# Performance work log

Hardware: AMD Instinct MI355X
Metric: run time of the kernel (lower is better)

The kernel has to match this reference:

```python
import jax, jax.numpy as jnp
import numpy as np

B, G, GI = 128, 360, 174          # batch, n_groups, voxels per group
EF, ET, U = 512, 512, 512         # feat embed, text embed, LSTM units
AU, VOC, T = 32, 5000, 20         # attention units, vocab, max_len


def _leaky(x):
    return jnp.where(x >= 0, x, 0.2 * x)


def _ln(x, g, b, eps=1e-5):
    m = x.mean(-1, keepdims=True)
    v = ((x - m) ** 2).mean(-1, keepdims=True)
    return (x - m) / jnp.sqrt(v + eps) * g + b


def setup_inputs() -> dict:
    key = jax.random.key(0)
    ks = jax.random.split(key, 24)
    def n(k, shape, s=0.02):
        return jax.random.normal(k, shape, jnp.float32) * s
    return {
        "features": jax.random.normal(ks[0], (B, G * GI), jnp.float32),
        "text": jax.random.randint(ks[1], (B, T), 0, VOC),
        "a0": jnp.zeros((B, U), jnp.float32),
        "c0": jnp.zeros((B, U), jnp.float32),
        "enc_W": n(ks[2], (G, GI, EF)), "enc_b": n(ks[3], (G, EF)),
        "enc_ln_g": jnp.ones((EF,), jnp.float32), "enc_ln_b": jnp.zeros((EF,), jnp.float32),
        "attn_W1": n(ks[4], (EF, AU)), "attn_b1": n(ks[5], (AU,)),
        "attn_W2": n(ks[6], (U, AU)), "attn_b2": n(ks[7], (AU,)),
        "attn_V": n(ks[8], (AU, 1)), "attn_bV": n(ks[9], (1,)),
        "emb": n(ks[10], (VOC, ET)),
        "W_ih": n(ks[11], (4 * U, EF + ET)), "W_hh": n(ks[12], (4 * U, U)),
        "b_ih": n(ks[13], (4 * U,)), "b_hh": n(ks[14], (4 * U,)),
        "ln_g": jnp.ones((U,), jnp.float32), "ln_b": jnp.zeros((U,), jnp.float32),
        "dec_W1": n(ks[15], (U, 256)), "dec_b1": n(ks[16], (256,)),
        "dec_W2": n(ks[17], (256, VOC)), "dec_b2": n(ks[18], (VOC,)),
        "subject": 0,
    }


def reference(features, text, a0, c0, enc_W, enc_b, enc_ln_g, enc_ln_b,
              attn_W1, attn_b1, attn_W2, attn_b2, attn_V, attn_bV, emb,
              W_ih, W_hh, b_ih, b_hh, ln_g, ln_b,
              dec_W1, dec_b1, dec_W2, dec_b2, subject):
    # LocallyConnected encoder (weights for the selected subject): groups are
    # 360 contiguous equal splits of the voxel axis -> gather == reshape.
    x = features.reshape(B, G, GI)
    feat = _ln(_leaky(jnp.einsum('bgi,gio->bgo', x, enc_W) + enc_b),
               enc_ln_g, enc_ln_b)                       # [B, G, EF]
    # hidden-independent half of attention, hoisted out of the recurrence
    f1 = jax.nn.relu(jnp.einsum('bge,eu->bgu', feat, attn_W1) + attn_b1)  # [B,G,AU]
    txt = emb[text]                                      # [B, T, ET]

    def step(carry, x_t):
        a, c = carry                                     # [B,U], [B,U]
        h2 = jax.nn.relu(a @ attn_W2 + attn_b2)          # [B, AU]
        score = jnp.tanh(f1 + h2[:, None, :]) @ attn_V + attn_bV  # [B,G,1]
        w = jax.nn.softmax(score, axis=1)
        ctx = jnp.sum(w * feat, axis=1)                  # [B, EF]
        xin = jnp.concatenate([ctx, x_t], axis=1)        # [B, EF+ET]
        gates = xin @ W_ih.T + a @ W_hh.T + b_ih + b_hh  # [B, 4U]
        i, f, g, o = jnp.split(gates, 4, axis=1)         # torch gate order i,f,g,o
        c = jax.nn.sigmoid(f) * c + jax.nn.sigmoid(i) * jnp.tanh(g)
        h = jax.nn.sigmoid(o) * jnp.tanh(c)
        a = _ln(_leaky(h), ln_g, ln_b)                   # fed back as LSTM hidden
        out = jax.nn.softmax(_leaky(a @ dec_W1 + dec_b1) @ dec_W2 + dec_b2, axis=-1)
        return (a, c), (out, w)

    _, (outs, ws) = jax.lax.scan(step, (a0, c0), jnp.swapaxes(txt, 0, 1))
    output = jnp.swapaxes(outs, 0, 1)                    # [B, T, VOC]
    attention_scores = jnp.swapaxes(ws, 0, 1)            # [B, T, G, 1]
    return output, attention_scores
```

## Files before the change

### kernel.cpp

```cpp
#include <hip/hip_runtime.h>
#include <stdint.h>

#define B_  128
#define G_  360
#define GI_ 174
#define EF_ 512
#define U_  512
#define AU_ 32
#define VOC_ 5000
#define T_  20

typedef short short8 __attribute__((ext_vector_type(8)));
typedef float floatx4 __attribute__((ext_vector_type(4)));

#define GLD16(gp, lp) __builtin_amdgcn_global_load_lds( \
    (const __attribute__((address_space(1))) void*)(gp), \
    (__attribute__((address_space(3))) void*)(lp), 16, 0, 0)

__device__ __forceinline__ unsigned short f2bf(float f){
  unsigned u = __float_as_uint(f);
  u += 0x7fffu + ((u>>16)&1u);
  return (unsigned short)(u>>16);
}
__device__ __forceinline__ float2 bfpair(unsigned u){
  float2 r; r.x = __uint_as_float(u<<16); r.y = __uint_as_float(u & 0xffff0000u); return r;
}
__device__ __forceinline__ unsigned packbf(float a, float b){
  return ((unsigned)f2bf(b)<<16) | (unsigned)f2bf(a);
}
__device__ __forceinline__ float sigmf(float x){ return 1.0f/(1.0f + __expf(-x)); }
__device__ __forceinline__ float tanhf_(float x){ return 1.0f - 2.0f/(1.0f + __expf(2.0f*x)); }
__device__ __forceinline__ float leaky_(float x){ return x >= 0.f ? x : 0.2f*x; }

__device__ __forceinline__ int swzcol(int cc, int e){
  return (cc & ~63) | ((((cc>>3)&7) ^ e)<<3) | (cc&7);
}

__global__ __launch_bounds__(256) void k_cvt(
    const int* __restrict__ text, const float* __restrict__ emb,
    const float* __restrict__ Wih, const float* __restrict__ Whh,
    const float* __restrict__ bih, const float* __restrict__ bhh,
    const float* __restrict__ W1, const float* __restrict__ b1,
    const float* __restrict__ encg, const float* __restrict__ encb,
    const float* __restrict__ dW1, const float* __restrict__ dW2,
    float* __restrict__ stats, unsigned short* __restrict__ Wstep,
    float* __restrict__ bias_sum, unsigned short* __restrict__ ASbuf,
    unsigned short* __restrict__ W1g, float* __restrict__ f1c,
    unsigned short* __restrict__ dW1t, unsigned short* __restrict__ dW2t)
{
  __shared__ float tile[64][65];
  const int blk = blockIdx.x, tid = threadIdx.x;
  if (blk < 90){
    int i = blk*1024 + tid*4;
    *(float4*)&stats[i] = make_float4(0.f,0.f,0.f,0.f);
  } else if (blk < 346){
    int j = (blk - 90)*8 + (tid >> 5);
    int e = j & 7;
    #pragma unroll
    for (int z=0; z<6; ++z){
      int c0 = ((tid & 31) + 32*z)*8;
      float4 v0, v1;
      if (c0 < 512){
        v0 = *(const float4*)&Wih[(size_t)j*1024 + 512 + c0];
        v1 = *(const float4*)&Wih[(size_t)j*1024 + 512 + c0 + 4];
      } else if (c0 < 1024){
        v0 = *(const float4*)&Wih[(size_t)j*1024 + (c0 - 512)];
        v1 = *(const float4*)&Wih[(size_t)j*1024 + (c0 - 512) + 4];
      } else {
        v0 = *(const float4*)&Whh[(size_t)j*512 + (c0 - 1024)];
        v1 = *(const float4*)&Whh[(size_t)j*512 + (c0 - 1024) + 4];
      }
      uint4 pk;
      pk.x = packbf(v0.x, v0.y); pk.y = packbf(v0.z, v0.w);
      pk.z = packbf(v1.x, v1.y); pk.w = packbf(v1.z, v1.w);
      int cd0;
      if (c0 < 512) cd0 = c0;
      else {
        int cc = c0 - 512;
        cd0 = 512 + ((cc & ~63) | ((((cc>>3)&7) ^ e)<<3));
      }
      *(uint4*)&Wstep[(size_t)j*1536 + cd0] = pk;
    }
  } else if (blk < 354){
    int i = (blk-346)*256 + tid;
    bias_sum[i] = bih[i] + bhh[i];
  } else if (blk < 2914){
    int r = blk - 354; int t = r >> 7, b = r & 127;
    int idx = text[b*T_ + t];
    float2 v = *(const float2*)&emb[(size_t)idx*512 + 2*tid];
    ((unsigned*)ASbuf)[(((size_t)r*1536)>>1) + tid] = packbf(v.x, v.y);
  } else if (blk == 2914){
    if (tid < 32){
      float gw = 0.f, bw = 0.f;
      for (int k=0;k<512;++k){
        float wv = W1[(size_t)k*32 + tid];
        float gk = encg[k], bk = encb[k];
        W1g[(size_t)tid*512 + k] = f2bf(gk*wv);
        gw += gk*wv; bw += bk*wv;
      }
      f1c[tid] = gw; f1c[32+tid] = bw + b1[tid];
    }
  } else if (blk < 2947){
    int q = blk - 2915; int kt = q >> 2, nt = q & 3;
    int k0 = kt*64, n0 = nt*64;
    #pragma unroll
    for (int it=0; it<16; ++it){
      int idx = it*256 + tid; int kk = idx>>6, nn = idx&63;
      tile[kk][nn] = dW1[(size_t)(k0+kk)*256 + n0+nn];
    }
    __syncthreads();
    #pragma unroll
    for (int it=0; it<16; ++it){
      int idx = it*256 + tid; int nn = idx>>6, kk = idx&63;
      dW1t[(size_t)(n0+nn)*512 + k0+kk] = f2bf(tile[kk][nn]);
    }
  } else {
    int q = blk - 2947; int kt = q/80, nt = q - kt*80;
    int k0 = kt*64, n0 = nt*64;
    #pragma unroll
    for (int it=0; it<16; ++it){
      int idx = it*256 + tid; int kk = idx>>6, nn = idx&63;
      tile[kk][nn] = (n0+nn < VOC_) ? dW2[(size_t)(k0+kk)*VOC_ + n0+nn] : 0.f;
    }
    __syncthreads();
    #pragma unroll
    for (int it=0; it<16; ++it){
      int idx = it*256 + tid; int nn = idx>>6, kk = idx&63;
      dW2t[(size_t)(n0+nn)*256 + k0+kk] = f2bf(tile[kk][nn]);
    }
  }
}

__device__ __forceinline__ int swz64(int row, int k){
  return row*64 + ((((k>>3) ^ (row&7)))<<3) + (k&7);
}
__global__ __launch_bounds__(256) void k_enc(
    const float* __restrict__ features, const float* __restrict__ encW,
    const float* __restrict__ encB,
    unsigned short* __restrict__ ybuf, float* __restrict__ stats)
{
  __shared__ __align__(16) unsigned short As[64*64];
  __shared__ __align__(16) unsigned short Bs[64*64];
  const int g = blockIdx.y;
  const int m0 = (blockIdx.x >> 3)*64, n0 = (blockIdx.x & 7)*64;
  const int tid = threadIdx.x, w = tid>>6, l = tid&63;
  const int quad = l>>4, col16 = l&15;
  const int m0w = (w>>1)*32, n0w = (w&1)*32;

  floatx4 acc[2][2];
  #pragma unroll
  for (int mi=0;mi<2;++mi)
    #pragma unroll
    for (int ni=0;ni<2;++ni)
      acc[mi][ni] = (floatx4){0.f,0.f,0.f,0.f};

  for (int c=0; c<3; ++c){
    if (c > 0) __syncthreads();
    #pragma unroll
    for (int q=0; q<4; ++q){
      int idx = q*256 + tid;
      int row = idx >> 4;
      int kl  = (idx & 15)*4;
      int kgl = c*64 + kl;
      const float* fp = features + (size_t)(m0+row)*(G_*GI_) + (size_t)g*GI_ + kgl;
      float4 v;
      if (kgl + 3 < GI_){
        v = *(const float4*)fp;
      } else {
        v.x = (kgl+0 < GI_) ? fp[0] : 0.f;
        v.y = (kgl+1 < GI_) ? fp[1] : 0.f;
        v.z = (kgl+2 < GI_) ? fp[2] : 0.f;
        v.w = (kgl+3 < GI_) ? fp[3] : 0.f;
      }
      int e = row*64 + (((kl>>3) ^ (row&7))<<3) + (kl&7);
      uint2 pk; pk.x = packbf(v.x, v.y); pk.y = packbf(v.z, v.w);
      *(uint2*)&As[e] = pk;
    }
    #pragma unroll
    for (int z=0; z<8; ++z){
      int kk = (tid>>5) + 8*z;
      int k  = c*64 + kk;
      int nn = (tid&31)*2;
      if (k < GI_){
        const float* wp = encW + ((size_t)g*GI_ + k)*512 + n0 + nn;
        float2 v = *(const float2*)wp;
        Bs[swz64(nn,   kk)] = f2bf(v.x);
        Bs[swz64(nn+1, kk)] = f2bf(v.y);
      } else {
        Bs[swz64(nn,   kk)] = 0;
        Bs[swz64(nn+1, kk)] = 0;
      }
    }
    __syncthreads();
    #pragma unroll
    for (int it=0; it<2; ++it){
      int kk = it*32 + quad*8;
      short8 af[2], bfr[2];
      #pragma unroll
      for (int mi=0;mi<2;++mi){
        int row = m0w + mi*16 + col16;
        af[mi] = *(const short8*)&As[row*64 + (((kk>>3) ^ (row&7))<<3)];
      }
      #pragma unroll
      for (int ni=0;ni<2;++ni){
        int rowb = n0w + ni*16 + col16;
        bfr[ni] = *(const short8*)&Bs[rowb*64 + (((kk>>3) ^ (rowb&7))<<3)];
      }
      #pragma unroll
      for (int mi=0;mi<2;++mi)
        #pragma unroll
        for (int ni=0;ni<2;++ni)
          acc[mi][ni] = __builtin_amdgcn_mfma_f32_16x16x32_bf16(af[mi], bfr[ni], acc[mi][ni], 0,0,0);
    }
  }

  #pragma unroll
  for (int mi=0;mi<2;++mi){
    float sy[4] = {0.f,0.f,0.f,0.f};
    float sq[4] = {0.f,0.f,0.f,0.f};
    #pragma unroll
    for (int ni=0;ni<2;++ni){
      int nG = n0 + n0w + ni*16 + col16;
      float bv = encB[(size_t)g*512 + nG];
      #pragma unroll
      for (int reg=0;reg<4;++reg){
        int row = m0 + m0w + mi*16 + quad*4 + reg;
        float y = leaky_(acc[mi][ni][reg] + bv);
        unsigned short yh = f2bf(y);
        ybuf[((size_t)row*G_ + g)*512 + nG] = yh;
        float yr = __uint_as_float(((unsigned)yh)<<16);
        sy[reg] += yr; sq[reg] += yr*yr;
      }
    }
    #pragma unroll
    for (int reg=0; reg<4; ++reg){
      float a = sy[reg], bq = sq[reg];
      #pragma unroll
      for (int mk=1; mk<16; mk<<=1){ a += __shfl_xor(a, mk, 64); bq += __shfl_xor(bq, mk, 64); }
      if (col16 == 0){
        int row = m0 + m0w + mi*16 + quad*4 + reg;
        atomicAdd(&stats[((size_t)row*G_ + g)*2],     a);
        atomicAdd(&stats[((size_t)row*G_ + g)*2 + 1], bq);
      }
    }
  }
}

template<int TN, int NBK, int MODE, int KSPLIT=1>
__global__ __launch_bounds__(256) void k_gemm(
    const unsigned short* __restrict__ A, int lda,
    const unsigned short* __restrict__ Bt, int ldb,
    const float* __restrict__ bias,
    float* __restrict__ outf, unsigned short* __restrict__ outh,
    const float* __restrict__ stats, float* __restrict__ stats2,
    const float* __restrict__ f1c)
{
  constexpr int NI = TN/32;
  __shared__ __align__(16) unsigned short As[128*64];
  __shared__ __align__(16) unsigned short Bs[TN*64];
  const int tid = threadIdx.x;
  const int w = tid >> 6, l = tid & 63;
  const int n0 = blockIdx.x * TN;
  const int ks = (KSPLIT > 1) ? blockIdx.y : 0;
  const int r0 = (KSPLIT > 1) ? 0 : blockIdx.y * 128;
  const int quad = l>>4, col16 = l&15;
  const int m0w = (w>>1)*64, n0w = (w&1)*(TN/2);
  const int arow = w*32, brow = w*(TN/4);

  const unsigned short* Ag = A + (size_t)(r0 + arow + (l>>3))*lda + (l&7)*8;
  const unsigned short* Bg = Bt + (size_t)(n0 + brow + (l>>3))*ldb + (l&7)*8;

  floatx4 acc[4][NI];
  #pragma unroll
  for (int mi=0;mi<4;++mi)
    #pragma unroll
    for (int ni=0;ni<NI;++ni)
      acc[mi][ni] = (floatx4){0.f,0.f,0.f,0.f};

  for (int it=0; it<NBK; ++it){
    int k0 = (ks*NBK + it)*64;
    #pragma unroll
    for (int q=0;q<4;++q)
      GLD16(Ag + (size_t)q*8*lda + k0, As + (arow + q*8)*64);
    #pragma unroll
    for (int q=0;q<TN/32;++q)
      GLD16(Bg + (size_t)q*8*ldb + k0, Bs + (brow + q*8)*64);
    __syncthreads();
    #pragma unroll
    for (int kc=0;kc<2;++kc){
      int koff = kc*32 + quad*8;
      short8 af[4], bfr[NI];
      #pragma unroll
      for (int mi=0;mi<4;++mi)
        af[mi] = *(const short8*)&As[(m0w + mi*16 + col16)*64 + koff];
      #pragma unroll
      for (int ni=0;ni<NI;++ni)
        bfr[ni] = *(const short8*)&Bs[(n0w + ni*16 + col16)*64 + koff];
      #pragma unroll
      for (int mi=0;mi<4;++mi)
        #pragma unroll
        for (int ni=0;ni<NI;++ni)
          acc[mi][ni] = __builtin_amdgcn_mfma_f32_16x16x32_bf16(af[mi], bfr[ni], acc[mi][ni], 0,0,0);
    }
    __syncthreads();
  }

  if constexpr (MODE == 0){
    float* op = outf + (size_t)ks*(128*2048);
    #pragma unroll
    for (int ni=0; ni<NI; ++ni){
      int nG = n0 + n0w + ni*16 + col16;
      float bv = (KSPLIT == 1 || ks == 0) ? bias[nG] : 0.f;
      #pragma unroll
      for (int mi=0; mi<4; ++mi)
        #pragma unroll
        for (int reg=0; reg<4; ++reg){
          int r = r0 + m0w + mi*16 + quad*4 + reg;
          op[(size_t)r*2048 + nG] = acc[mi][ni][reg] + bv;
        }
    }
  } else if constexpr (MODE == 1){
    int nG = n0w + col16;
    float gw = f1c[nG], bwv = f1c[32+nG];
    #pragma unroll
    for (int mi=0; mi<4; ++mi)
      #pragma unroll
      for (int reg=0; reg<4; ++reg){
        int r = r0 + m0w + mi*16 + quad*4 + reg;
        float2 st = *(const float2*)&stats[(size_t)r*2];
        float m = st.x * (1.f/512.f);
        float var = st.y * (1.f/512.f) - m*m;
        float rs = rsqrtf(var + 1e-5f);
        float v = rs*(acc[mi][0][reg] - m*gw) + bwv;
        v = v > 0.f ? v : 0.f;
        outf[(size_t)r*32 + nG] = v;
        if (((w&1)==0) && col16==0){
          stats2[(size_t)r*2] = m; stats2[(size_t)r*2+1] = rs;
        }
      }
  } else if constexpr (MODE == 2){
    #pragma unroll
    for (int ni=0; ni<NI; ++ni){
      int nG = n0 + n0w + ni*16 + col16;
      float bv = bias[nG];
      #pragma unroll
      for (int mi=0; mi<4; ++mi)
        #pragma unroll
        for (int reg=0; reg<4; ++reg){
          int r = r0 + m0w + mi*16 + quad*4 + reg;
          outh[(size_t)r*256 + nG] = f2bf(leaky_(acc[mi][ni][reg] + bv));
        }
    }
  } else {
    #pragma unroll
    for (int ni=0; ni<NI; ++ni){
      int nG = n0 + n0w + ni*16 + col16;
      if (nG < VOC_){
        float bv = bias[nG];
        #pragma unroll
        for (int mi=0; mi<4; ++mi)
          #pragma unroll
          for (int reg=0; reg<4; ++reg){
            int r = r0 + m0w + mi*16 + quad*4 + reg;
            int bb = r & 127, tt = r >> 7;
            outf[((size_t)bb*T_ + tt)*VOC_ + nG] = acc[mi][ni][reg] + bv;
          }
      }
    }
  }
}

__global__ __launch_bounds__(256) void k_gates(
    const unsigned short* __restrict__ A,
    const unsigned short* __restrict__ Bt,
    float* __restrict__ outp)
{
  __shared__ __align__(16) unsigned short As[128*128];
  __shared__ __align__(16) unsigned short Bs[64*128];
  const int tid = threadIdx.x, w = tid>>6, l = tid&63;
  const int ks = blockIdx.y;
  const int n0 = blockIdx.x*64;
  const int quad = l>>4, col16 = l&15;
  const int m0w = (w>>1)*64, n0w = (w&1)*32;
  const int arow = w*32, brow = w*16;

  const unsigned short* Ag = A + (size_t)(arow + (l>>4))*1536 + ks*128 + (l&15)*8;
  const unsigned short* Bg = Bt + (size_t)(n0 + brow + (l>>4))*1536 + 512 + ks*128 + (l&15)*8;
  #pragma unroll
  for (int q=0;q<8;++q)
    GLD16(Ag + (size_t)q*4*1536, As + (arow + q*4)*128);
  #pragma unroll
  for (int q=0;q<4;++q)
    GLD16(Bg + (size_t)q*4*1536, Bs + (brow + q*4)*128);

  floatx4 acc[4][2];
  #pragma unroll
  for (int mi=0;mi<4;++mi)
    #pragma unroll
    for (int ni=0;ni<2;++ni)
      acc[mi][ni] = (floatx4){0.f,0.f,0.f,0.f};

  __syncthreads();
  #pragma unroll
  for (int kc=0;kc<4;++kc){
    int koff = kc*32 + quad*8;
    int kbase = koff & 64;
    int kx = (koff>>3)&7;
    short8 af[4], bfr[2];
    #pragma unroll
    for (int mi=0;mi<4;++mi){
      int row = m0w + mi*16 + col16;
      af[mi] = *(const short8*)&As[row*128 + kbase + ((kx ^ (row&7))<<3)];
    }
    #pragma unroll
    for (int ni=0;ni<2;++ni){
      int rowb = n0w + ni*16 + col16;
      bfr[ni] = *(const short8*)&Bs[rowb*128 + kbase + ((kx ^ (rowb&7))<<3)];
    }
    #pragma unroll
    for (int mi=0;mi<4;++mi)
      #pragma unroll
      for (int ni=0;ni<2;++ni)
        acc[mi][ni] = __builtin_amdgcn_mfma_f32_16x16x32_bf16(af[mi], bfr[ni], acc[mi][ni], 0,0,0);
  }

  float* op = outp + (size_t)ks*(128*2048);
  #pragma unroll
  for (int ni=0; ni<2; ++ni){
    int nG = n0 + n0w + ni*16 + col16;
    #pragma unroll
    for (int mi=0; mi<4; ++mi)
      #pragma unroll
      for (int reg=0; reg<4; ++reg){
        int r = m0w + mi*16 + quad*4 + reg;
        op[(size_t)r*2048 + nG] = acc[mi][ni][reg];
      }
  }
}

__global__ __launch_bounds__(256) void k_cellattn(
    const float* __restrict__ gall, const float* __restrict__ gtx,
    const float* __restrict__ c_in,
    float* __restrict__ c_out, const float* __restrict__ a0,
    const float* __restrict__ lng, const float* __restrict__ lnb,
    const float* __restrict__ W2, const float* __restrict__ b2,
    const float* __restrict__ Vv, const float* __restrict__ bV,
    const float* __restrict__ f1, const unsigned short* __restrict__ ybuf,
    const float* __restrict__ stats2,
    const float* __restrict__ encg, const float* __restrict__ encb,
    unsigned short* __restrict__ ASlot, unsigned short* __restrict__ a_bf,
    float* __restrict__ att_out, int t_att, int mode_cell, int do_attn)
{
  __shared__ float a_s[512];
  __shared__ float sc[G_];
  __shared__ float hred[8*32];
  __shared__ float h2s[32];
  __shared__ float red[16];
  __shared__ float mrs[2];
  __shared__ float2 cred[4][256];
  const int b = blockIdx.x, tid = threadIdx.x;
  const int wv = tid >> 6, ln = tid & 63;

  if (mode_cell){
    float hl2[2];
    #pragma unroll
    for (int q=0;q<2;++q){
      int u = tid + q*256;
      size_t base = (size_t)b*2048;
      float gi = gtx[base+u];
      float gf = gtx[base+512+u];
      float gc = gtx[base+1024+u];
      float go = gtx[base+1536+u];
      #pragma unroll
      for (int s=0;s<8;++s){
        const float* gp = gall + (size_t)s*(128*2048) + base;
        gi += gp[u]; gf += gp[512+u]; gc += gp[1024+u]; go += gp[1536+u];
      }
      float c = sigmf(gf)*c_in[(size_t)b*512+u] + sigmf(gi)*tanhf_(gc);
      c_out[(size_t)b*512+u] = c;
      hl2[q] = leaky_(sigmf(go)*tanhf_(c));
    }
    float s = hl2[0]+hl2[1], ss = hl2[0]*hl2[0]+hl2[1]*hl2[1];
    #pragma unroll
    for (int mk=1;mk<64;mk<<=1){ s += __shfl_xor(s,mk,64); ss += __shfl_xor(ss,mk,64); }
    if (ln==0){ red[wv]=s; red[8+wv]=ss; }
    __syncthreads();
    if (tid==0){
      float S  = red[0]+red[1]+red[2]+red[3];
      float SS = red[8]+red[9]+red[10]+red[11];
      float mean = S*(1.f/512.f);
      float var  = SS*(1.f/512.f) - mean*mean;
      mrs[0]=mean; mrs[1]=rsqrtf(var+1e-5f);
    }
    __syncthreads();
    float mean = mrs[0], rstd = mrs[1];
    #pragma unroll
    for (int q=0;q<2;++q){
      int u = tid + q*256;
      float av = (hl2[q]-mean)*rstd*lng[u] + lnb[u];
      a_s[u] = av;
      a_bf[(size_t)b*512 + u] = f2bf(av);
      if (do_attn){
        int pc = swzcol(512 + u, b&7);
        ASlot[(size_t)b*1536 + 512 + pc] = f2bf(av);
      }
    }
  } else {
    #pragma unroll
    for (int q=0;q<2;++q){
      int u = tid + q*256;
      float av = a0[(size_t)b*512 + u];
      a_s[u] = av;
      int pc = swzcol(512 + u, b&7);
      ASlot[(size_t)b*1536 + 512 + pc] = f2bf(av);
    }
  }
  __syncthreads();
  if (!do_attn) return;

  {
    int u = tid & 31, ch = tid >> 5;
    float p = 0.f;
    const float* w2p = W2 + (size_t)ch*64*32 + u;
    const float* ap = a_s + ch*64;
    #pragma unroll 8
    for (int e=0;e<64;++e) p += ap[e]*w2p[(size_t)e*32];
    hred[ch*32+u] = p;
  }
  __syncthreads();
  if (tid < 32){
    float p = hred[tid];
    #pragma unroll
    for (int ch=1; ch<8; ++ch) p += hred[ch*32+tid];
    p += b2[tid];
    h2s[tid] = p>0.f? p:0.f;
  }
  __syncthreads();
  float bVv = bV[0];
  for (int gg = tid; gg < G_; gg += 256){
    const float* fp = f1 + ((size_t)b*G_ + gg)*32;
    float s = bVv;
    #pragma unroll
    for (int u=0;u<32;++u) s += tanhf_(fp[u] + h2s[u]) * Vv[u];
    sc[gg] = s;
  }
  __syncthreads();
  float mx = -1e30f;
  for (int gg=tid; gg<G_; gg+=256) mx = fmaxf(mx, sc[gg]);
  #pragma unroll
  for (int mk=1;mk<64;mk<<=1) mx = fmaxf(mx, __shfl_xor(mx,mk,64));
  if (ln==0) red[wv]=mx;
  __syncthreads();
  if (tid==0) red[0] = fmaxf(fmaxf(red[0],red[1]),fmaxf(red[2],red[3]));
  __syncthreads();
  mx = red[0];
  float psum = 0.f;
  for (int gg=tid; gg<G_; gg+=256){
    float e = __expf(sc[gg]-mx);
    sc[gg] = e; psum += e;
  }
  #pragma unroll
  for (int mk=1;mk<64;mk<<=1) psum += __shfl_xor(psum,mk,64);
  if (ln==0) red[8+wv]=psum;
  __syncthreads();
  if (tid==0) red[8] = red[8]+red[9]+red[10]+red[11];
  __syncthreads();
  float inv = 1.f/red[8];
  float Mop = 0.f;
  float* wout = att_out + ((size_t)b*T_ + t_att)*G_;
  for (int gg=tid; gg<G_; gg+=256){
    float wg = sc[gg]*inv;
    wout[gg] = wg;
    float2 st = *(const float2*)&stats2[((size_t)b*G_+gg)*2];
    sc[gg] = wg*st.y;
    Mop += wg*st.x*st.y;
  }
  #pragma unroll
  for (int mk=1;mk<64;mk<<=1) Mop += __shfl_xor(Mop,mk,64);
  if (ln==0) red[4+wv] = Mop;
  __syncthreads();
  if (tid==0) mrs[0] = red[4]+red[5]+red[6]+red[7];
  __syncthreads();
  float Mo = mrs[0];
  {
    const unsigned* fp = (const unsigned*)ybuf + ((size_t)b*G_)*256;
    float2 cacc[4];
    #pragma unroll
    for (int k=0;k<4;++k) cacc[k] = make_float2(0.f,0.f);
    int g0 = wv*90;
    for (int gg=g0; gg<g0+90; ++gg){
      float wq = sc[gg];
      #pragma unroll
      for (int k=0;k<4;++k){
        float2 p = bfpair(fp[(size_t)gg*256 + ln + 64*k]);
        cacc[k].x += wq*p.x; cacc[k].y += wq*p.y;
      }
    }
    #pragma unroll
    for (int k=0;k<4;++k) cred[wv][ln + 64*k] = cacc[k];
  }
  __syncthreads();
  {
    float c0v = cred[0][tid].x + cred[1][tid].x + cred[2][tid].x + cred[3][tid].x;
    float c1v = cred[0][tid].y + cred[1][tid].y + cred[2][tid].y + cred[3][tid].y;
    int e0 = 2*tid;
    float ctx0 = encg[e0]  *(c0v - Mo) + encb[e0];
    float ctx1 = encg[e0+1]*(c1v - Mo) + encb[e0+1];
    int pc = swzcol(2*tid, b&7);
    ((unsigned*)ASlot)[((size_t)b*1536 + 512 + pc)>>1] = packbf(ctx0, ctx1);
  }
}

__global__ __launch_bounds__(256) void k_softmax(float* __restrict__ outp)
{
  __shared__ float red[8];
  const size_t row = (size_t)blockIdx.x * VOC_;
  const int tid = threadIdx.x;
  const int wv = tid >> 6, ln = tid & 63;
  float v[20];
  float mx = -1e30f;
  #pragma unroll
  for (int k=0;k<20;++k){
    int idx = tid + k*256;
    v[k] = (idx < VOC_) ? outp[row+idx] : -1e30f;
    mx = fmaxf(mx, v[k]);
  }
  #pragma unroll
  for (int mk=1;mk<64;mk<<=1) mx = fmaxf(mx,__shfl_xor(mx,mk,64));
  if (ln==0) red[wv] = mx;
  __syncthreads();
  if (tid==0) red[0]=fmaxf(fmaxf(red[0],red[1]),fmaxf(red[2],red[3]));
  __syncthreads();
  mx = red[0];
  float s=0.f;
  #pragma unroll
  for (int k=0;k<20;++k){ v[k] = __expf(v[k]-mx); s += v[k]; }
  #pragma unroll
  for (int mk=1;mk<64;mk<<=1) s += __shfl_xor(s,mk,64);
  if (ln==0) red[4+wv]=s;
  __syncthreads();
  if (tid==0) red[4]=red[4]+red[5]+red[6]+red[7];
  __syncthreads();
  float inv = 1.f/red[4];
  #pragma unroll
  for (int k=0;k<20;++k){
    int idx = tid + k*256;
    if (idx < VOC_) outp[row+idx] = v[k]*inv;
  }
}

extern "C" void kernel_launch(void* const* d_in, const int* in_sizes, int n_in,
                              void* d_out, int out_size, void* d_ws, size_t ws_size,
                              hipStream_t stream) {
  const float* features = (const float*)d_in[0];
  const int*   text     = (const int*)d_in[1];
  const float* a0    = (const float*)d_in[2];
  const float* c0    = (const float*)d_in[3];
  const float* encW  = (const float*)d_in[4];
  const float* encB  = (const float*)d_in[5];
  const float* encLNg= (const float*)d_in[6];
  const float* encLNb= (const float*)d_in[7];
  const float* attnW1= (const float*)d_in[8];
  const float* attnb1= (const float*)d_in[9];
  const float* attnW2= (const float*)d_in[10];
  const float* attnb2= (const float*)d_in[11];
  const float* attnV = (const float*)d_in[12];
  const float* attnbV= (const float*)d_in[13];
  const float* emb   = (const float*)d_in[14];
  const float* Wih   = (const float*)d_in[15];
  const float* Whh   = (const float*)d_in[16];
  const float* bih   = (const float*)d_in[17];
  const float* bhh   = (const float*)d_in[18];
  const float* lng   = (const float*)d_in[19];
  const float* lnb   = (const float*)d_in[20];
  const float* dW1   = (const float*)d_in[21];
  const float* db1   = (const float*)d_in[22];
  const float* dW2   = (const float*)d_in[23];
  const float* db2   = (const float*)d_in[24];

  uint8_t* w8 = (uint8_t*)d_ws;
  unsigned short* ybuf   = (unsigned short*)(w8);
  float*          stats  = (float*)(w8 + 47185920);
  float*          stats2 = (float*)(w8 + 47554560);
  float*          f1b    = (float*)(w8 + 47923200);
  unsigned short* ASbuf  = (unsigned short*)(w8 + 53821440);
  unsigned short* Wstep  = (unsigned short*)(w8 + 61685760);
  float*          bias_sum=(float*)(w8 + 67977216);
  unsigned short* W1g    = (unsigned short*)(w8 + 67985408);
  float*          f1c    = (float*)(w8 + 68018176);
  unsigned short* dW1t   = (unsigned short*)(w8 + 68018432);
  unsigned short* dW2t   = (unsigned short*)(w8 + 68280576);
  float*          cws    = (float*)(w8 + 71950592);
  unsigned short* a_bf   = (unsigned short*)(w8 + 72212736);
  unsigned short* d1bf   = (unsigned short*)(w8 + 74834176);

  float* outp = (float*)d_out;
  float* att  = outp + 12800000;
  float* gsplit = outp;
  float* gtxt   = outp + 8*128*2048;

  hipLaunchKernelGGL(k_cvt, dim3(3267), dim3(256), 0, stream,
                     text, emb, Wih, Whh, bih, bhh, attnW1, attnb1,
                     encLNg, encLNb, dW1, dW2,
                     stats, Wstep, bias_sum, ASbuf, W1g, f1c, dW1t, dW2t);
  hipLaunchKernelGGL(k_enc, dim3(16,360), dim3(256), 0, stream,
                     features, encW, encB, ybuf, stats);
  hipLaunchKernelGGL((k_gemm<64,8,0>), dim3(32,20), dim3(256), 0, stream,
                     ASbuf, 1536, Wstep, 1536, bias_sum,
                     gtxt, (unsigned short*)nullptr,
                     (const float*)nullptr, (float*)nullptr, (const float*)nullptr);
  hipLaunchKernelGGL((k_gemm<32,8,1>), dim3(1,360), dim3(256), 0, stream,
                     ybuf, 512, W1g, 512, (const float*)nullptr,
                     f1b, (unsigned short*)nullptr, stats, stats2, f1c);
  hipLaunchKernelGGL(k_cellattn, dim3(128), dim3(256), 0, stream,
                     gsplit, gtxt, c0, cws, a0, lng, lnb, attnW2, attnb2, attnV, attnbV,
                     f1b, ybuf, stats2, encLNg, encLNb,
                     ASbuf, a_bf, att, 0, 0, 1);
  for (int t=0; t<T_; ++t){
    hipLaunchKernelGGL(k_gates, dim3(32,8), dim3(256), 0, stream,
                       ASbuf + (size_t)t*128*1536 + 512, Wstep, gsplit);
    int da = (t < T_-1) ? 1 : 0;
    unsigned short* slot = ASbuf + (size_t)((t+1 < T_) ? (t+1) : 0)*128*1536;
    hipLaunchKernelGGL(k_cellattn, dim3(128), dim3(256), 0, stream,
                       gsplit, gtxt + (size_t)t*128*2048, (t==0)?c0:cws, cws, a0, lng, lnb,
                       attnW2, attnb2, attnV, attnbV,
                       f1b, ybuf, stats2, encLNg, encLNb,
                       slot, a_bf + (size_t)t*128*512, att, t+1, 1, da);
  }
  hipLaunchKernelGGL((k_gemm<128,8,2>), dim3(2,20), dim3(256), 0, stream,
                     a_bf, 512, dW1t, 512, db1,
                     (float*)nullptr, d1bf, (const float*)nullptr, (float*)nullptr,
                     (const float*)nullptr);
  hipLaunchKernelGGL((k_gemm<128,4,3>), dim3(40,20), dim3(256), 0, stream,
                     d1bf, 256, dW2t, 256, db2,
                     outp, (unsigned short*)nullptr, (const float*)nullptr,
                     (float*)nullptr, (const float*)nullptr);
  hipLaunchKernelGGL(k_softmax, dim3(2560), dim3(256), 0, stream, outp);
}
```

Measured before the change: 1.069 ms.

## Widen encoder GEMM tiles and add optional pre-converted bf16 encoder weights

The encoder GEMM now uses 512-thread blocks that cover all 128 batch rows and 128 output columns per group, instead of 64x64 tiles. This cuts how many times the features and encoder weights are re-read from global memory. When the workspace is large enough, a new pass in the conversion kernel pre-converts encW to a swizzled bf16 layout, and the encoder then loads it straight into LDS with global_load_lds; otherwise it falls back to the fp32 path. The extra pass adds its own read/write traffic, which may offset part of the gain. The context loop in the cell/attention kernel also gets an unroll-2 hint.

```diff
diff --git a/kernel.cpp b/kernel.cpp
--- a/kernel.cpp
+++ b/kernel.cpp
@@ -43,10 +43,12 @@
     const float* __restrict__ W1, const float* __restrict__ b1,
     const float* __restrict__ encg, const float* __restrict__ encb,
     const float* __restrict__ dW1, const float* __restrict__ dW2,
+    const float* __restrict__ encW,
     float* __restrict__ stats, unsigned short* __restrict__ Wstep,
     float* __restrict__ bias_sum, unsigned short* __restrict__ ASbuf,
     unsigned short* __restrict__ W1g, float* __restrict__ f1c,
-    unsigned short* __restrict__ dW1t, unsigned short* __restrict__ dW2t)
+    unsigned short* __restrict__ dW1t, unsigned short* __restrict__ dW2t,
+    unsigned short* __restrict__ encWbf)
 {
   __shared__ float tile[64][65];
   const int blk = blockIdx.x, tid = threadIdx.x;
@@ -114,7 +116,7 @@
       int idx = it*256 + tid; int nn = idx>>6, kk = idx&63;
       dW1t[(size_t)(n0+nn)*512 + k0+kk] = f2bf(tile[kk][nn]);
     }
-  } else {
+  } else if (blk < 3267){
     int q = blk - 2947; int kt = q/80, nt = q - kt*80;
     int k0 = kt*64, n0 = nt*64;
     #pragma unroll
@@ -128,41 +130,103 @@
       int idx = it*256 + tid; int nn = idx>>6, kk = idx&63;
       dW2t[(size_t)(n0+nn)*256 + k0+kk] = f2bf(tile[kk][nn]);
     }
+  } else {
+    int q = blk - 3267;
+    int g = q >> 3, nt = q & 7;
+    int n0 = nt*64;
+    for (int c=0; c<3; ++c){
+      if (c) __syncthreads();
+      #pragma unroll
+      for (int it=0; it<16; ++it){
+        int idx = it*256 + tid; int kk = idx>>6, nn = idx&63;
+        int k = c*64 + kk;
+        tile[kk][nn] = (k < GI_) ? encW[((size_t)g*GI_ + k)*512 + n0 + nn] : 0.f;
+      }
+      __syncthreads();
+      #pragma unroll
+      for (int r=0; r<2; ++r){
+        int u = r*256 + tid;
+        int nn = u >> 3, pb = u & 7;
+        int kb = pb ^ (nn & 7);
+        uint4 pk;
+        pk.x = packbf(tile[kb*8+0][nn], tile[kb*8+1][nn]);
+        pk.y = packbf(tile[kb*8+2][nn], tile[kb*8+3][nn]);
+        pk.z = packbf(tile[kb*8+4][nn], tile[kb*8+5][nn]);
+        pk.w = packbf(tile[kb*8+6][nn], tile[kb*8+7][nn]);
+        *(uint4*)&encWbf[((size_t)g*512 + n0 + nn)*192 + c*64 + pb*8] = pk;
+      }
+    }
   }
 }
 
 __device__ __forceinline__ int swz64(int row, int k){
   return row*64 + ((((k>>3) ^ (row&7)))<<3) + (k&7);
 }
-__global__ __launch_bounds__(256) void k_enc(
+
+__device__ __forceinline__ void enc_epilogue(
+    floatx4 (&acc)[2][4], const float* encB, unsigned short* ybuf,
+    float* stats, int g, int n0, int n0w, int m0w, int quad, int col16)
+{
+  #pragma unroll
+  for (int mi=0;mi<2;++mi){
+    float sy[4] = {0.f,0.f,0.f,0.f};
+    float sq[4] = {0.f,0.f,0.f,0.f};
+    #pragma unroll
+    for (int ni=0;ni<4;++ni){
+      int nG = n0 + n0w + ni*16 + col16;
+      float bv = encB[(size_t)g*512 + nG];
+      #pragma unroll
+      for (int reg=0;reg<4;++reg){
+        int row = m0w + mi*16 + quad*4 + reg;
+        float y = leaky_(acc[mi][ni][reg] + bv);
+        unsigned short yh = f2bf(y);
+        ybuf[((size_t)row*G_ + g)*512 + nG] = yh;
+        float yr = __uint_as_float(((unsigned)yh)<<16);
+        sy[reg] += yr; sq[reg] += yr*yr;
+      }
+    }
+    #pragma unroll
+    for (int reg=0; reg<4; ++reg){
+      float a = sy[reg], bq = sq[reg];
+      #pragma unroll
+      for (int mk=1; mk<16; mk<<=1){ a += __shfl_xor(a, mk, 64); bq += __shfl_xor(bq, mk, 64); }
+      if (col16 == 0){
+        int row = m0w + mi*16 + quad*4 + reg;
+        atomicAdd(&stats[((size_t)row*G_ + g)*2],     a);
+        atomicAdd(&stats[((size_t)row*G_ + g)*2 + 1], bq);
+      }
+    }
+  }
+}
+
+__global__ __launch_bounds__(512) void k_enc_f32(
     const float* __restrict__ features, const float* __restrict__ encW,
     const float* __restrict__ encB,
     unsigned short* __restrict__ ybuf, float* __restrict__ stats)
 {
-  __shared__ __align__(16) unsigned short As[64*64];
-  __shared__ __align__(16) unsigned short Bs[64*64];
-  const int g = blockIdx.y;
-  const int m0 = (blockIdx.x >> 3)*64, n0 = (blockIdx.x & 7)*64;
+  __shared__ __align__(16) unsigned short As[128*64];
+  __shared__ __align__(16) unsigned short Bs[128*64];
+  const int g = blockIdx.y, n0 = blockIdx.x*128;
   const int tid = threadIdx.x, w = tid>>6, l = tid&63;
   const int quad = l>>4, col16 = l&15;
-  const int m0w = (w>>1)*32, n0w = (w&1)*32;
-
-  floatx4 acc[2][2];
+  const int m0w = (w>>1)*32, n0w = (w&1)*64;
+
+  floatx4 acc[2][4];
   #pragma unroll
   for (int mi=0;mi<2;++mi)
     #pragma unroll
-    for (int ni=0;ni<2;++ni)
+    for (int ni=0;ni<4;++ni)
       acc[mi][ni] = (floatx4){0.f,0.f,0.f,0.f};
 
   for (int c=0; c<3; ++c){
     if (c > 0) __syncthreads();
     #pragma unroll
     for (int q=0; q<4; ++q){
-      int idx = q*256 + tid;
+      int idx = q*512 + tid;
       int row = idx >> 4;
       int kl  = (idx & 15)*4;
       int kgl = c*64 + kl;
-      const float* fp = features + (size_t)(m0+row)*(G_*GI_) + (size_t)g*GI_ + kgl;
+      const float* fp = features + (size_t)row*(G_*GI_) + (size_t)g*GI_ + kgl;
       float4 v;
       if (kgl + 3 < GI_){
         v = *(const float4*)fp;
@@ -178,9 +242,9 @@
     }
     #pragma unroll
     for (int z=0; z<8; ++z){
-      int kk = (tid>>5) + 8*z;
+      int kk = (tid>>6) + 8*z;
       int k  = c*64 + kk;
-      int nn = (tid&31)*2;
+      int nn = (tid&63)*2;
       if (k < GI_){
         const float* wp = encW + ((size_t)g*GI_ + k)*512 + n0 + nn;
         float2 v = *(const float2*)wp;
@@ -195,55 +259,97 @@
     #pragma unroll
     for (int it=0; it<2; ++it){
       int kk = it*32 + quad*8;
-      short8 af[2], bfr[2];
+      short8 af[2], bfr[4];
       #pragma unroll
       for (int mi=0;mi<2;++mi){
         int row = m0w + mi*16 + col16;
         af[mi] = *(const short8*)&As[row*64 + (((kk>>3) ^ (row&7))<<3)];
       }
       #pragma unroll
-      for (int ni=0;ni<2;++ni){
+      for (int ni=0;ni<4;++ni){
         int rowb = n0w + ni*16 + col16;
         bfr[ni] = *(const short8*)&Bs[rowb*64 + (((kk>>3) ^ (rowb&7))<<3)];
       }
       #pragma unroll
       for (int mi=0;mi<2;++mi)
         #pragma unroll
-        for (int ni=0;ni<2;++ni)
+        for (int ni=0;ni<4;++ni)
           acc[mi][ni] = __builtin_amdgcn_mfma_f32_16x16x32_bf16(af[mi], bfr[ni], acc[mi][ni], 0,0,0);
     }
   }
-
-  #pragma unroll
-  for (int mi=0;mi<2;++mi){
-    float sy[4] = {0.f,0.f,0.f,0.f};
-    float sq[4] = {0.f,0.f,0.f,0.f};
-    #pragma unroll
-    for (int ni=0;ni<2;++ni){
-      int nG = n0 + n0w + ni*16 + col16;
-      float bv = encB[(size_t)g*512 + nG];
-      #pragma unroll
-      for (int reg=0;reg<4;++reg){
-        int row = m0 + m0w + mi*16 + quad*4 + reg;
-        float y = leaky_(acc[mi][ni][reg] + bv);
-        unsigned short yh = f2bf(y);
-        ybuf[((size_t)row*G_ + g)*512 + nG] = yh;
-        float yr = __uint_as_float(((unsigned)yh)<<16);
-        sy[reg] += yr; sq[reg] += yr*yr;
-      }
-    }
-    #pragma unroll
-    for (int reg=0; reg<4; ++reg){
-      float a = sy[reg], bq = sq[reg];
-      #pragma unroll
-      for (int mk=1; mk<16; mk<<=1){ a += __shfl_xor(a, mk, 64); bq += __shfl_xor(bq, mk, 64); }
-      if (col16 == 0){
-        int row = m0 + m0w + mi*16 + quad*4 + reg;
-        atomicAdd(&stats[((size_t)row*G_ + g)*2],     a);
-        atomicAdd(&stats[((size_t)row*G_ + g)*2 + 1], bq);
-      }
-    }
-  }
+  enc_epilogue(acc, encB, ybuf, stats, g, n0, n0w, m0w, quad, col16);
+}
+
+__global__ __launch_bounds__(512) void k_enc_bf(
+    const float* __restrict__ features, const unsigned short* __restrict__ encWbf,
+    const float* __restrict__ encB,
+    unsigned short* __restrict__ ybuf, float* __restrict__ stats)
+{
+  __shared__ __align__(16) unsigned short As[128*64];
+  __shared__ __align__(16) unsigned short Bs[128*64];
+  const int g = blockIdx.y, n0 = blockIdx.x*128;
+  const int tid = threadIdx.x, w = tid>>6, l = tid&63;
+  const int quad = l>>4, col16 = l&15;
+  const int m0w = (w>>1)*32, n0w = (w&1)*64;
+  const int brow = w*16;
+
+  const unsigned short* Bg = encWbf + ((size_t)g*512 + n0 + brow + (l>>3))*192 + (l&7)*8;
+
+  floatx4 acc[2][4];
+  #pragma unroll
+  for (int mi=0;mi<2;++mi)
+    #pragma unroll
+    for (int ni=0;ni<4;++ni)
+      acc[mi][ni] = (floatx4){0.f,0.f,0.f,0.f};
+
+  for (int c=0; c<3; ++c){
+    if (c > 0) __syncthreads();
+    #pragma unroll
+    for (int q=0;q<2;++q)
+      GLD16(Bg + (size_t)q*8*192 + c*64, Bs + (brow + q*8)*64);
+    #pragma unroll
+    for (int q=0; q<4; ++q){
+      int idx = q*512 + tid;
+      int row = idx >> 4;
+      int kl  = (idx & 15)*4;
+      int kgl = c*64 + kl;
+      const float* fp = features + (size_t)row*(G_*GI_) + (size_t)g*GI_ + kgl;
+      float4 v;
+      if (kgl + 3 < GI_){
+        v = *(const float4*)fp;
+      } else {
+        v.x = (kgl+0 < GI_) ? fp[0] : 0.f;
+        v.y = (kgl+1 < GI_) ? fp[1] : 0.f;
+        v.z = (kgl+2 < GI_) ? fp[2] : 0.f;
+        v.w = (kgl+3 < GI_) ? fp[3] : 0.f;
+      }
+      int e = row*64 + (((kl>>3) ^ (row&7))<<3) + (kl&7);
+      uint2 pk; pk.x = packbf(v.x, v.y); pk.y = packbf(v.z, v.w);
+      *(uint2*)&As[e] = pk;
+    }
+    __syncthreads();
+    #pragma unroll
+    for (int it=0; it<2; ++it){
+      int kk = it*32 + quad*8;
+      short8 af[2], bfr[4];
+      #pragma unroll
+      for (int mi=0;mi<2;++mi){
+        int row = m0w + mi*16 + col16;
+        af[mi] = *(const short8*)&As[row*64 + (((kk>>3) ^ (row&7))<<3)];
+      }
+      #pragma unroll
+      for (int ni=0;ni<4;++ni){
+        int rowb = n0w + ni*16 + col16;
+        bfr[ni] = *(const short8*)&Bs[rowb*64 + (((kk>>3) ^ (rowb&7))<<3)];
+      }
+      #pragma unroll
+      for (int mi=0;mi<2;++mi)
+        #pragma unroll
+        for (int ni=0;ni<4;++ni)
+          acc[mi][ni] = __builtin_amdgcn_mfma_f32_16x16x32_bf16(af[mi], bfr[ni], acc[mi][ni], 0,0,0);
+    }
+  }
+  enc_epilogue(acc, encB, ybuf, stats, g, n0, n0w, m0w, quad, col16);
 }
 
 template<int TN, int NBK, int MODE, int KSPLIT=1>
@@ -588,6 +694,7 @@
     #pragma unroll
     for (int k=0;k<4;++k) cacc[k] = make_float2(0.f,0.f);
     int g0 = wv*90;
+    #pragma unroll 2
     for (int gg=g0; gg<g0+90; ++gg){
       float wq = sc[gg];
       #pragma unroll
@@ -693,18 +800,27 @@
   float*          cws    = (float*)(w8 + 71950592);
   unsigned short* a_bf   = (unsigned short*)(w8 + 72212736);
   unsigned short* d1bf   = (unsigned short*)(w8 + 74834176);
+  const size_t ENCBF_OFF = 76144896;
+  const size_t ENCBF_SZ  = 70778880;
+  unsigned short* encWbf = (unsigned short*)(w8 + ENCBF_OFF);
+  const bool use_bf = (ws_size >= ENCBF_OFF + ENCBF_SZ);
 
   float* outp = (float*)d_out;
   float* att  = outp + 12800000;
   float* gsplit = outp;
   float* gtxt   = outp + 8*128*2048;
 
-  hipLaunchKernelGGL(k_cvt, dim3(3267), dim3(256), 0, stream,
+  hipLaunchKernelGGL(k_cvt, dim3(use_bf ? 6147 : 3267), dim3(256), 0, stream,
                      text, emb, Wih, Whh, bih, bhh, attnW1, attnb1,
-                     encLNg, encLNb, dW1, dW2,
-                     stats, Wstep, bias_sum, ASbuf, W1g, f1c, dW1t, dW2t);
-  hipLaunchKernelGGL(k_enc, dim3(16,360), dim3(256), 0, stream,
-                     features, encW, encB, ybuf, stats);
+                     encLNg, encLNb, dW1, dW2, encW,
+                     stats, Wstep, bias_sum, ASbuf, W1g, f1c, dW1t, dW2t,
+                     encWbf);
+  if (use_bf)
+    hipLaunchKernelGGL(k_enc_bf, dim3(4,360), dim3(512), 0, stream,
+                       features, encWbf, encB, ybuf, stats);
+  else
+    hipLaunchKernelGGL(k_enc_f32, dim3(4,360), dim3(512), 0, stream,
+                       features, encW, encB, ybuf, stats);
   hipLaunchKernelGGL((k_gemm<64,8,0>), dim3(32,20), dim3(256), 0, stream,
                      ASbuf, 1536, Wstep, 1536, bias_sum,
                      gtxt, (unsigned short*)nullptr,
```

Result: slower. 1.202 ms (+12.4%).
